# Kernel tuning notes

Measured on AMD Instinct MI355X. Metric: run time of the kernel, lower is better.

The kernel has to match this reference:

```python
import jax, jax.numpy as jnp
import numpy as np

B, H, W = 8, 56, 56
DIM, DIM_OUT, NUM_HEADS = 96, 192, 3
Q_STRIDE = (2, 2)


def setup_inputs() -> dict:
    key = jax.random.key(0)
    k1, k2, k3 = jax.random.split(key, 3)
    x = jax.random.normal(k1, (B, H, W, DIM), dtype=jnp.float32)
    W_qkv = jax.random.normal(k2, (DIM, 3 * DIM_OUT), dtype=jnp.float32) * 0.02
    b_qkv = jnp.zeros((3 * DIM_OUT,), dtype=jnp.float32)
    W_proj = jax.random.normal(k3, (DIM_OUT, DIM_OUT), dtype=jnp.float32) * 0.02
    b_proj = jnp.zeros((DIM_OUT,), dtype=jnp.float32)
    return {"x": x, "W_qkv": W_qkv, "b_qkv": b_qkv, "W_proj": W_proj, "b_proj": b_proj}


def reference(x, W_qkv, b_qkv, W_proj, b_proj):
    b, h, w, _ = x.shape
    c = W_proj.shape[0]          # dim_out
    nh = NUM_HEADS
    hd = c // nh                 # head_dim
    sh, sw = Q_STRIDE

    # fused QKV projection: (B,H,W,3*C)
    qkv = jnp.einsum("bhwd,de->bhwe", x, W_qkv) + b_qkv
    qkv = qkv.reshape(b, h * w, 3, nh, hd)
    q, k, v = qkv[:, :, 0], qkv[:, :, 1], qkv[:, :, 2]  # each (B,N,nh,hd)

    # query max-pool over spatial dims (channels = nh*hd, heads interleaved as in original)
    q = q.reshape(b, h, w, c)
    q = q.reshape(b, h // sh, sh, w // sw, sw, c).max(axis=(2, 4))  # (B,H',W',C)
    hn, wn = h // sh, w // sw
    q = q.reshape(b, hn * wn, nh, hd)

    # heads-first layout, scaled q
    q = q.transpose(0, 2, 1, 3) / jnp.sqrt(jnp.asarray(hd, x.dtype))  # (B,nh,Nq,hd)
    k = k.transpose(0, 2, 1, 3)                                       # (B,nh,Nk,hd)
    v = v.transpose(0, 2, 1, 3)

    attn = jax.nn.softmax(jnp.einsum("bnqd,bnkd->bnqk", q, k), axis=-1)
    out = jnp.einsum("bnqk,bnkd->bnqd", attn, v)        # (B,nh,Nq,hd)
    out = out.transpose(0, 2, 1, 3).reshape(b, hn, wn, c)

    return jnp.einsum("bhwc,cd->bhwd", out, W_proj) + b_proj
```

## Files before the change

### kernel.cpp

```cpp
#include <hip/hip_runtime.h>

#define BB    8
#define E3    576
#define DIMO  192
#define NH    3
#define HD    64
#define NK    3136
#define NQ    784
#define M1    25088
#define M2    6272
#define KSPLIT 7
#define KSLICE 448

typedef __bf16 bf16x8 __attribute__((ext_vector_type(8)));
typedef float f32x4  __attribute__((ext_vector_type(4)));

__device__ inline unsigned short f2bf(float f) {
    unsigned int u = __builtin_bit_cast(unsigned int, f);
    u += 0x7FFFu + ((u >> 16) & 1u);
    return (unsigned short)(u >> 16);
}

__global__ void wb_kernel(const float* __restrict__ Wqkv, unsigned short* __restrict__ Wb) {
    __shared__ float Ls[96][33];
    const int t = threadIdx.x;
    const int n0 = blockIdx.x * 32;
    int rr = t >> 5, c = t & 31;
#pragma unroll
    for (int rb = 0; rb < 12; ++rb) {
        int row = rb * 8 + rr;
        Ls[row][c] = Wqkv[(size_t)row * 576 + n0 + c];
    }
    __syncthreads();
    int n = t >> 3, kc = (t & 7) * 12;
#pragma unroll
    for (int j = 0; j < 12; j += 4) {
        ushort4 u = { f2bf(Ls[kc + j][n]), f2bf(Ls[kc + j + 1][n]),
                      f2bf(Ls[kc + j + 2][n]), f2bf(Ls[kc + j + 3][n]) };
        *(ushort4*)(Wb + (size_t)(n0 + n) * 96 + kc + j) = u;
    }
}

__launch_bounds__(256)
__global__ void qkv_mfma(const float* __restrict__ x,
                         const unsigned short* __restrict__ Wb,
                         const float* __restrict__ bias,
                         float* __restrict__ Qtmp,
                         unsigned short* __restrict__ Kb,
                         unsigned short* __restrict__ Vt) {
    __shared__ unsigned short xs[64 * 104];
    const int tid = threadIdx.x;
    const int wave = tid >> 6, lane = tid & 63;
    const int quad = lane >> 4, l16 = lane & 15;
    const int ntile = blockIdx.x;
    const int m0 = blockIdx.y * 64;

#pragma unroll
    for (int i = 0; i < 6; ++i) {
        int f = tid + i * 256;
        int r = f / 24, c4 = f % 24;
        float4 v = ((const float4*)x)[(size_t)(m0 + r) * 24 + c4];
        ushort4 u = { f2bf(v.x), f2bf(v.y), f2bf(v.z), f2bf(v.w) };
        *(ushort4*)&xs[r * 104 + c4 * 4] = u;
    }
    __syncthreads();

    f32x4 acc[12];
#pragma unroll
    for (int i = 0; i < 12; ++i) acc[i] = (f32x4){0.f, 0.f, 0.f, 0.f};

    const unsigned short* wb = Wb + (size_t)(ntile * 192 + l16) * 96 + quad * 8;
#pragma unroll
    for (int ch = 0; ch < 3; ++ch) {
        bf16x8 af = *(const bf16x8*)&xs[(wave * 16 + l16) * 104 + ch * 32 + quad * 8];
#pragma unroll
        for (int nf = 0; nf < 12; ++nf) {
            bf16x8 bfr = *(const bf16x8*)(wb + (size_t)nf * 16 * 96 + ch * 32);
            acc[nf] = __builtin_amdgcn_mfma_f32_16x16x32_bf16(af, bfr, acc[nf], 0, 0, 0);
        }
    }

    const int mbase = m0 + wave * 16 + quad * 4;
    if (ntile == 0) {
#pragma unroll
        for (int nf = 0; nf < 12; ++nf) {
            int n = nf * 16 + l16;
            float bs = bias[n];
#pragma unroll
            for (int i = 0; i < 4; ++i)
                Qtmp[(size_t)(mbase + i) * 192 + n] = acc[nf][i] + bs;
        }
    } else if (ntile == 1) {
#pragma unroll
        for (int nf = 0; nf < 12; ++nf) {
            int n = nf * 16 + l16;
            float bs = bias[192 + n];
#pragma unroll
            for (int i = 0; i < 4; ++i)
                Kb[(size_t)(mbase + i) * 192 + n] = f2bf(acc[nf][i] + bs);
        }
    } else {
        int b = m0 / NK;
        int key = mbase - b * NK;
#pragma unroll
        for (int nf = 0; nf < 12; ++nf) {
            int n = nf * 16 + l16;
            float bs = bias[384 + n];
            int hh = n >> 6, dd = n & 63;
            ushort4 u = { f2bf(acc[nf][0] + bs), f2bf(acc[nf][1] + bs),
                          f2bf(acc[nf][2] + bs), f2bf(acc[nf][3] + bs) };
            *(ushort4*)(Vt + ((size_t)((b * 3 + hh) * 64 + dd)) * NK + key) = u;
        }
    }
}

__global__ void qpool_bf16(const float* __restrict__ Qtmp, unsigned short* __restrict__ Qpb) {
    int idx = blockIdx.x * 256 + threadIdx.x;
    int d  = idx & 63;
    int q  = (idx >> 6) % NQ;
    int bh = idx / (64 * NQ);
    int b = bh / NH, h = bh % NH;
    int hq = q / 28, wq = q % 28;
    const float* base = Qtmp + (size_t)b * NK * 192 + h * 64 + d;
    int r0 = (2 * hq) * 56 + 2 * wq;
    float m = base[(size_t)r0 * 192];
    m = fmaxf(m, base[(size_t)(r0 + 1) * 192]);
    m = fmaxf(m, base[(size_t)(r0 + 56) * 192]);
    m = fmaxf(m, base[(size_t)(r0 + 57) * 192]);
    Qpb[idx] = f2bf(m * 0.125f);
}

__launch_bounds__(256)
__global__ void attn_mfma(const unsigned short* __restrict__ Qpb,
                          const unsigned short* __restrict__ Kb,
                          const unsigned short* __restrict__ Vt,
                          float* __restrict__ Pnum,
                          float* __restrict__ Pden) {
    __shared__ unsigned short Ks[64 * 88];
    __shared__ unsigned short Vs[64 * 88];
    __shared__ unsigned short Ps[4 * 32 * 88];

    const int tid = threadIdx.x;
    const int wave = tid >> 6, lane = tid & 63;
    const int quad = lane >> 4, l16 = lane & 15;
    const int bh = blockIdx.y, b = bh / NH, h = bh % NH;
    const int qt = blockIdx.x * 128 + wave * 32;
    const int ks = blockIdx.z, k00 = ks * KSLICE;

    const int srow0 = tid >> 3, sch = (tid & 7) * 8;
    const unsigned short* kg  = Kb + ((size_t)(b * NK + k00) + srow0) * DIMO + h * 64 + sch;
    const unsigned short* kg1 = kg + (size_t)32 * DIMO;
    const unsigned short* vg  = Vt + ((size_t)bh * 64 + srow0) * NK + k00 + sch;
    const unsigned short* vg1 = vg + (size_t)32 * NK;

    uint4 kp0 = *(const uint4*)kg;
    uint4 kp1 = *(const uint4*)kg1;
    uint4 vp0 = *(const uint4*)vg;
    uint4 vp1 = *(const uint4*)vg1;

    int qa = min(qt + l16, NQ - 1);
    int qb = min(qt + 16 + l16, NQ - 1);
    const unsigned short* qpa = Qpb + ((size_t)bh * NQ + qa) * HD + quad * 8;
    const unsigned short* qpc = Qpb + ((size_t)bh * NQ + qb) * HD + quad * 8;
    bf16x8 qf[2][2];
    qf[0][0] = *(const bf16x8*)qpa;  qf[0][1] = *(const bf16x8*)(qpa + 32);
    qf[1][0] = *(const bf16x8*)qpc;  qf[1][1] = *(const bf16x8*)(qpc + 32);

    const __bf16 one = (__bf16)1.0f;
    bf16x8 ones = { one, one, one, one, one, one, one, one };

    f32x4 on[4][2];
#pragma unroll
    for (int i = 0; i < 4; ++i)
#pragma unroll
        for (int j = 0; j < 2; ++j) on[i][j] = (f32x4){0.f, 0.f, 0.f, 0.f};
    f32x4 dn[2];
    dn[0] = (f32x4){0.f, 0.f, 0.f, 0.f};
    dn[1] = (f32x4){0.f, 0.f, 0.f, 0.f};

    unsigned short* myP = Ps + wave * 32 * 88;

    for (int s = 0; s < 7; ++s) {
        __syncthreads();
        *(uint4*)&Ks[srow0 * 88 + sch]        = kp0;
        *(uint4*)&Ks[(srow0 + 32) * 88 + sch] = kp1;
        *(uint4*)&Vs[srow0 * 88 + sch]        = vp0;
        *(uint4*)&Vs[(srow0 + 32) * 88 + sch] = vp1;
        __syncthreads();
        if (s < 6) {
            kp0 = *(const uint4*)(kg  + (size_t)(s + 1) * 64 * DIMO);
            kp1 = *(const uint4*)(kg1 + (size_t)(s + 1) * 64 * DIMO);
            vp0 = *(const uint4*)(vg  + (s + 1) * 64);
            vp1 = *(const uint4*)(vg1 + (s + 1) * 64);
        }

#pragma unroll
        for (int ksub = 0; ksub < 4; ++ksub) {
            bf16x8 kf0 = *(const bf16x8*)&Ks[(ksub * 16 + l16) * 88 + quad * 8];
            bf16x8 kf1 = *(const bf16x8*)&Ks[(ksub * 16 + l16) * 88 + 32 + quad * 8];
#pragma unroll
            for (int qsub = 0; qsub < 2; ++qsub) {
                f32x4 sa = (f32x4){0.f, 0.f, 0.f, 0.f};
                sa = __builtin_amdgcn_mfma_f32_16x16x32_bf16(kf0, qf[qsub][0], sa, 0, 0, 0);
                sa = __builtin_amdgcn_mfma_f32_16x16x32_bf16(kf1, qf[qsub][1], sa, 0, 0, 0);
                ushort4 pw = { f2bf(__expf(sa[0])), f2bf(__expf(sa[1])),
                               f2bf(__expf(sa[2])), f2bf(__expf(sa[3])) };
                *(ushort4*)&myP[(qsub * 16 + l16) * 88 + ksub * 16 + quad * 4] = pw;
            }
        }

#pragma unroll
        for (int k32 = 0; k32 < 2; ++k32) {
            bf16x8 pf0 = *(const bf16x8*)&myP[l16 * 88 + k32 * 32 + quad * 8];
            bf16x8 pf1 = *(const bf16x8*)&myP[(16 + l16) * 88 + k32 * 32 + quad * 8];
            dn[0] = __builtin_amdgcn_mfma_f32_16x16x32_bf16(ones, pf0, dn[0], 0, 0, 0);
            dn[1] = __builtin_amdgcn_mfma_f32_16x16x32_bf16(ones, pf1, dn[1], 0, 0, 0);
#pragma unroll
            for (int dsub = 0; dsub < 4; ++dsub) {
                bf16x8 vf = *(const bf16x8*)&Vs[(dsub * 16 + l16) * 88 + k32 * 32 + quad * 8];
                on[dsub][0] = __builtin_amdgcn_mfma_f32_16x16x32_bf16(vf, pf0, on[dsub][0], 0, 0, 0);
                on[dsub][1] = __builtin_amdgcn_mfma_f32_16x16x32_bf16(vf, pf1, on[dsub][1], 0, 0, 0);
            }
        }
    }

#pragma unroll
    for (int qsub = 0; qsub < 2; ++qsub) {
        int q = qt + qsub * 16 + l16;
        if (q < NQ) {
            size_t base = (size_t)ks * (24 * NQ * HD) + ((size_t)bh * NQ + q) * HD + quad * 4;
#pragma unroll
            for (int dsub = 0; dsub < 4; ++dsub)
                *(f32x4*)(Pnum + base + dsub * 16) = on[dsub][qsub];
            if (quad == 0) Pden[ks * (24 * NQ) + bh * NQ + q] = dn[qsub][0];
        }
    }
}

__global__ void combine_kernel(const float* __restrict__ Pnum,
                               const float* __restrict__ Pden,
                               float* __restrict__ AO) {
    int idx = blockIdx.x * 256 + threadIdx.x;
    int d = idx & 63;
    int rest = idx >> 6;
    int qq = rest % NQ;
    int bh = rest / NQ;
    int b = bh / NH, h = bh % NH;
    float num = 0.f, den = 0.f;
#pragma unroll
    for (int s = 0; s < KSPLIT; ++s) {
        num += Pnum[(size_t)s * (24 * NQ * HD) + idx];
        den += Pden[s * (24 * NQ) + bh * NQ + qq];
    }
    AO[((size_t)b * NQ + qq) * DIMO + h * 64 + d] = num / den;
}

template<int K, int LDB>
__launch_bounds__(256)
__global__ void gemm_kernel(const float* __restrict__ A,
                            const float* __restrict__ B,
                            const float* __restrict__ bias,
                            float* __restrict__ C) {
    constexpr int KT = 96;
    __shared__ float As[32][KT + 4];
    __shared__ float Bs[KT][64];

    const int tid = threadIdx.x;
    const int bm = blockIdx.y * 32;
    const int bn = blockIdx.x * 64;
    const int tx = tid & 15;
    const int ty = tid >> 4;

    float4 acc0 = {0.f, 0.f, 0.f, 0.f};
    float4 acc1 = {0.f, 0.f, 0.f, 0.f};

    for (int k0 = 0; k0 < K; k0 += KT) {
#pragma unroll
        for (int i = 0; i < 3; ++i) {
            int f = tid + i * 256;
            int r = f / 24, c = f % 24;
            float4 v = ((const float4*)A)[(size_t)(bm + r) * (K / 4) + (k0 / 4) + c];
            ((float4*)&As[r][0])[c] = v;
        }
#pragma unroll
        for (int i = 0; i < 6; ++i) {
            int f = tid + i * 256;
            int r = f >> 4, c = f & 15;
            float4 v = ((const float4*)B)[(size_t)(k0 + r) * (LDB / 4) + (bn >> 2) + c];
            ((float4*)&Bs[r][0])[c] = v;
        }
        __syncthreads();

#pragma unroll 8
        for (int k = 0; k < KT; ++k) {
            float a0 = As[ty][k];
            float a1 = As[ty + 16][k];
            float4 bb = ((const float4*)&Bs[k][0])[tx];
            acc0.x = fmaf(a0, bb.x, acc0.x);
            acc0.y = fmaf(a0, bb.y, acc0.y);
            acc0.z = fmaf(a0, bb.z, acc0.z);
            acc0.w = fmaf(a0, bb.w, acc0.w);
            acc1.x = fmaf(a1, bb.x, acc1.x);
            acc1.y = fmaf(a1, bb.y, acc1.y);
            acc1.z = fmaf(a1, bb.z, acc1.z);
            acc1.w = fmaf(a1, bb.w, acc1.w);
        }
        __syncthreads();
    }

    float4 bb = ((const float4*)bias)[(bn >> 2) + tx];
    acc0.x += bb.x; acc0.y += bb.y; acc0.z += bb.z; acc0.w += bb.w;
    acc1.x += bb.x; acc1.y += bb.y; acc1.z += bb.z; acc1.w += bb.w;

    ((float4*)C)[(size_t)(bm + ty) * (LDB / 4) + (bn >> 2) + tx] = acc0;
    ((float4*)C)[(size_t)(bm + ty + 16) * (LDB / 4) + (bn >> 2) + tx] = acc1;
}

extern "C" void kernel_launch(void* const* d_in, const int* in_sizes, int n_in,
                              void* d_out, int out_size, void* d_ws, size_t ws_size,
                              hipStream_t stream) {
    const float* x     = (const float*)d_in[0];
    const float* Wqkv  = (const float*)d_in[1];
    const float* bqkv  = (const float*)d_in[2];
    const float* Wproj = (const float*)d_in[3];
    const float* bproj = (const float*)d_in[4];
    float* out = (float*)d_out;

    float* Qtmp = (float*)d_ws;
    float* Pnum = Qtmp + (size_t)M1 * 192;
    float* Pden = Pnum + (size_t)KSPLIT * 24 * NQ * HD;
    float* AO   = Pden + (size_t)KSPLIT * 24 * NQ;
    unsigned short* Qpb = (unsigned short*)(AO + (size_t)M2 * DIMO);
    unsigned short* Kb  = Qpb + (size_t)24 * NQ * HD;
    unsigned short* Vt  = Kb + (size_t)BB * NK * DIMO;
    unsigned short* Wb  = Vt + (size_t)24 * HD * NK;

    wb_kernel<<<18, 256, 0, stream>>>(Wqkv, Wb);

    qkv_mfma<<<dim3(3, M1 / 64), 256, 0, stream>>>(x, Wb, bqkv, Qtmp, Kb, Vt);

    qpool_bf16<<<(24 * NQ * HD) / 256, 256, 0, stream>>>(Qtmp, Qpb);

    attn_mfma<<<dim3(7, 24, KSPLIT), 256, 0, stream>>>(Qpb, Kb, Vt, Pnum, Pden);

    combine_kernel<<<(24 * NQ * HD) / 256, 256, 0, stream>>>(Pnum, Pden, AO);

    gemm_kernel<192, 192><<<dim3(3, 196), 256, 0, stream>>>(AO, Wproj, bproj, out);
}
```

Before: 148.4 us.

## Use bf16 MFMA for output projection and compute softmax denominator in registers

The fp32 scalar-FMA output projection GEMM is replaced by a bf16 MFMA kernel. The combine kernel now writes bf16 attention output, and a merged prep kernel converts W_proj to transposed bf16. In attention, the denominator is summed from fp32 exponentials in registers with a cross-lane shuffle instead of extra MFMAs against a ones vector. The P tile shrinks to a 32-column half with a smaller stride, so PV runs per half. This trades some precision in the projection for fewer instructions and smaller LDS use.

```diff
diff --git a/kernel.cpp b/kernel.cpp
--- a/kernel.cpp
+++ b/kernel.cpp
@@ -11,6 +11,7 @@
 #define M2    6272
 #define KSPLIT 7
 #define KSLICE 448
+#define PSTR  56
 
 typedef __bf16 bf16x8 __attribute__((ext_vector_type(8)));
 typedef float f32x4  __attribute__((ext_vector_type(4)));
@@ -21,23 +22,42 @@
     return (unsigned short)(u >> 16);
 }
 
-__global__ void wb_kernel(const float* __restrict__ Wqkv, unsigned short* __restrict__ Wb) {
-    __shared__ float Ls[96][33];
+__global__ void wprep(const float* __restrict__ Wqkv, const float* __restrict__ Wproj,
+                      unsigned short* __restrict__ Wb, unsigned short* __restrict__ Wpb) {
+    __shared__ float Ls[192][33];
     const int t = threadIdx.x;
-    const int n0 = blockIdx.x * 32;
-    int rr = t >> 5, c = t & 31;
-#pragma unroll
-    for (int rb = 0; rb < 12; ++rb) {
-        int row = rb * 8 + rr;
-        Ls[row][c] = Wqkv[(size_t)row * 576 + n0 + c];
-    }
-    __syncthreads();
-    int n = t >> 3, kc = (t & 7) * 12;
-#pragma unroll
-    for (int j = 0; j < 12; j += 4) {
-        ushort4 u = { f2bf(Ls[kc + j][n]), f2bf(Ls[kc + j + 1][n]),
-                      f2bf(Ls[kc + j + 2][n]), f2bf(Ls[kc + j + 3][n]) };
-        *(ushort4*)(Wb + (size_t)(n0 + n) * 96 + kc + j) = u;
+    if (blockIdx.x < 18) {
+        const int n0 = blockIdx.x * 32;
+        int rr = t >> 5, c = t & 31;
+#pragma unroll
+        for (int rb = 0; rb < 12; ++rb) {
+            int row = rb * 8 + rr;
+            Ls[row][c] = Wqkv[(size_t)row * 576 + n0 + c];
+        }
+        __syncthreads();
+        int n = t >> 3, kc = (t & 7) * 12;
+#pragma unroll
+        for (int j = 0; j < 12; j += 4) {
+            ushort4 u = { f2bf(Ls[kc + j][n]), f2bf(Ls[kc + j + 1][n]),
+                          f2bf(Ls[kc + j + 2][n]), f2bf(Ls[kc + j + 3][n]) };
+            *(ushort4*)(Wb + (size_t)(n0 + n) * 96 + kc + j) = u;
+        }
+    } else {
+        const int n0 = (blockIdx.x - 18) * 32;
+        int rr = t >> 5, c = t & 31;
+#pragma unroll
+        for (int rb = 0; rb < 24; ++rb) {
+            int row = rb * 8 + rr;
+            Ls[row][c] = Wproj[(size_t)row * 192 + n0 + c];
+        }
+        __syncthreads();
+        int n = t >> 3, kc = (t & 7) * 24;
+#pragma unroll
+        for (int j = 0; j < 24; j += 4) {
+            ushort4 u = { f2bf(Ls[kc + j][n]), f2bf(Ls[kc + j + 1][n]),
+                          f2bf(Ls[kc + j + 2][n]), f2bf(Ls[kc + j + 3][n]) };
+            *(ushort4*)(Wpb + (size_t)(n0 + n) * 192 + kc + j) = u;
+        }
     }
 }
 
@@ -48,7 +68,7 @@
                          float* __restrict__ Qtmp,
                          unsigned short* __restrict__ Kb,
                          unsigned short* __restrict__ Vt) {
-    __shared__ unsigned short xs[64 * 104];
+    __shared__ __attribute__((aligned(16))) unsigned short xs[64 * 104];
     const int tid = threadIdx.x;
     const int wave = tid >> 6, lane = tid & 63;
     const int quad = lane >> 4, l16 = lane & 15;
@@ -136,9 +156,9 @@
                           const unsigned short* __restrict__ Vt,
                           float* __restrict__ Pnum,
                           float* __restrict__ Pden) {
-    __shared__ unsigned short Ks[64 * 88];
-    __shared__ unsigned short Vs[64 * 88];
-    __shared__ unsigned short Ps[4 * 32 * 88];
+    __shared__ __attribute__((aligned(16))) unsigned short Ks[64 * 88];
+    __shared__ __attribute__((aligned(16))) unsigned short Vs[64 * 88];
+    __shared__ __attribute__((aligned(16))) unsigned short Ps[4 * 32 * PSTR];
 
     const int tid = threadIdx.x;
     const int wave = tid >> 6, lane = tid & 63;
@@ -166,19 +186,14 @@
     qf[0][0] = *(const bf16x8*)qpa;  qf[0][1] = *(const bf16x8*)(qpa + 32);
     qf[1][0] = *(const bf16x8*)qpc;  qf[1][1] = *(const bf16x8*)(qpc + 32);
 
-    const __bf16 one = (__bf16)1.0f;
-    bf16x8 ones = { one, one, one, one, one, one, one, one };
-
     f32x4 on[4][2];
 #pragma unroll
     for (int i = 0; i < 4; ++i)
 #pragma unroll
         for (int j = 0; j < 2; ++j) on[i][j] = (f32x4){0.f, 0.f, 0.f, 0.f};
-    f32x4 dn[2];
-    dn[0] = (f32x4){0.f, 0.f, 0.f, 0.f};
-    dn[1] = (f32x4){0.f, 0.f, 0.f, 0.f};
-
-    unsigned short* myP = Ps + wave * 32 * 88;
+    float dden0 = 0.f, dden1 = 0.f;
+
+    unsigned short* myP = Ps + wave * 32 * PSTR;
 
     for (int s = 0; s < 7; ++s) {
         __syncthreads();
@@ -195,29 +210,30 @@
         }
 
 #pragma unroll
-        for (int ksub = 0; ksub < 4; ++ksub) {
-            bf16x8 kf0 = *(const bf16x8*)&Ks[(ksub * 16 + l16) * 88 + quad * 8];
-            bf16x8 kf1 = *(const bf16x8*)&Ks[(ksub * 16 + l16) * 88 + 32 + quad * 8];
-#pragma unroll
-            for (int qsub = 0; qsub < 2; ++qsub) {
-                f32x4 sa = (f32x4){0.f, 0.f, 0.f, 0.f};
-                sa = __builtin_amdgcn_mfma_f32_16x16x32_bf16(kf0, qf[qsub][0], sa, 0, 0, 0);
-                sa = __builtin_amdgcn_mfma_f32_16x16x32_bf16(kf1, qf[qsub][1], sa, 0, 0, 0);
-                ushort4 pw = { f2bf(__expf(sa[0])), f2bf(__expf(sa[1])),
-                               f2bf(__expf(sa[2])), f2bf(__expf(sa[3])) };
-                *(ushort4*)&myP[(qsub * 16 + l16) * 88 + ksub * 16 + quad * 4] = pw;
+        for (int half = 0; half < 2; ++half) {
+#pragma unroll
+            for (int ksub = 0; ksub < 2; ++ksub) {
+                const int krow = (half * 32 + ksub * 16 + l16) * 88;
+                bf16x8 kf0 = *(const bf16x8*)&Ks[krow + quad * 8];
+                bf16x8 kf1 = *(const bf16x8*)&Ks[krow + 32 + quad * 8];
+#pragma unroll
+                for (int qsub = 0; qsub < 2; ++qsub) {
+                    f32x4 sa = (f32x4){0.f, 0.f, 0.f, 0.f};
+                    sa = __builtin_amdgcn_mfma_f32_16x16x32_bf16(kf0, qf[qsub][0], sa, 0, 0, 0);
+                    sa = __builtin_amdgcn_mfma_f32_16x16x32_bf16(kf1, qf[qsub][1], sa, 0, 0, 0);
+                    float p0 = __expf(sa[0]), p1 = __expf(sa[1]);
+                    float p2 = __expf(sa[2]), p3 = __expf(sa[3]);
+                    if (qsub == 0) dden0 += (p0 + p1) + (p2 + p3);
+                    else           dden1 += (p0 + p1) + (p2 + p3);
+                    ushort4 pw = { f2bf(p0), f2bf(p1), f2bf(p2), f2bf(p3) };
+                    *(ushort4*)&myP[(qsub * 16 + l16) * PSTR + ksub * 16 + quad * 4] = pw;
+                }
             }
-        }
-
-#pragma unroll
-        for (int k32 = 0; k32 < 2; ++k32) {
-            bf16x8 pf0 = *(const bf16x8*)&myP[l16 * 88 + k32 * 32 + quad * 8];
-            bf16x8 pf1 = *(const bf16x8*)&myP[(16 + l16) * 88 + k32 * 32 + quad * 8];
-            dn[0] = __builtin_amdgcn_mfma_f32_16x16x32_bf16(ones, pf0, dn[0], 0, 0, 0);
-            dn[1] = __builtin_amdgcn_mfma_f32_16x16x32_bf16(ones, pf1, dn[1], 0, 0, 0);
+            bf16x8 pf0 = *(const bf16x8*)&myP[l16 * PSTR + quad * 8];
+            bf16x8 pf1 = *(const bf16x8*)&myP[(16 + l16) * PSTR + quad * 8];
 #pragma unroll
             for (int dsub = 0; dsub < 4; ++dsub) {
-                bf16x8 vf = *(const bf16x8*)&Vs[(dsub * 16 + l16) * 88 + k32 * 32 + quad * 8];
+                bf16x8 vf = *(const bf16x8*)&Vs[(dsub * 16 + l16) * 88 + half * 32 + quad * 8];
                 on[dsub][0] = __builtin_amdgcn_mfma_f32_16x16x32_bf16(vf, pf0, on[dsub][0], 0, 0, 0);
                 on[dsub][1] = __builtin_amdgcn_mfma_f32_16x16x32_bf16(vf, pf1, on[dsub][1], 0, 0, 0);
             }
@@ -226,20 +242,23 @@
 
 #pragma unroll
     for (int qsub = 0; qsub < 2; ++qsub) {
+        float r = (qsub == 0) ? dden0 : dden1;
+        r += __shfl_xor(r, 16, 64);
+        r += __shfl_xor(r, 32, 64);
         int q = qt + qsub * 16 + l16;
         if (q < NQ) {
             size_t base = (size_t)ks * (24 * NQ * HD) + ((size_t)bh * NQ + q) * HD + quad * 4;
 #pragma unroll
             for (int dsub = 0; dsub < 4; ++dsub)
                 *(f32x4*)(Pnum + base + dsub * 16) = on[dsub][qsub];
-            if (quad == 0) Pden[ks * (24 * NQ) + bh * NQ + q] = dn[qsub][0];
+            if (quad == 0) Pden[ks * (24 * NQ) + bh * NQ + q] = r;
         }
     }
 }
 
 __global__ void combine_kernel(const float* __restrict__ Pnum,
                                const float* __restrict__ Pden,
-                               float* __restrict__ AO) {
+                               unsigned short* __restrict__ AObf) {
     int idx = blockIdx.x * 256 + threadIdx.x;
     int d = idx & 63;
     int rest = idx >> 6;
@@ -252,68 +271,53 @@
         num += Pnum[(size_t)s * (24 * NQ * HD) + idx];
         den += Pden[s * (24 * NQ) + bh * NQ + qq];
     }
-    AO[((size_t)b * NQ + qq) * DIMO + h * 64 + d] = num / den;
-}
-
-template<int K, int LDB>
+    AObf[((size_t)b * NQ + qq) * DIMO + h * 64 + d] = f2bf(num / den);
+}
+
 __launch_bounds__(256)
-__global__ void gemm_kernel(const float* __restrict__ A,
-                            const float* __restrict__ B,
-                            const float* __restrict__ bias,
-                            float* __restrict__ C) {
-    constexpr int KT = 96;
-    __shared__ float As[32][KT + 4];
-    __shared__ float Bs[KT][64];
-
+__global__ void proj_mfma(const unsigned short* __restrict__ AObf,
+                          const unsigned short* __restrict__ Wpb,
+                          const float* __restrict__ bproj,
+                          float* __restrict__ out) {
+    __shared__ __attribute__((aligned(16))) unsigned short as_[64 * 200];
     const int tid = threadIdx.x;
-    const int bm = blockIdx.y * 32;
-    const int bn = blockIdx.x * 64;
-    const int tx = tid & 15;
-    const int ty = tid >> 4;
-
-    float4 acc0 = {0.f, 0.f, 0.f, 0.f};
-    float4 acc1 = {0.f, 0.f, 0.f, 0.f};
-
-    for (int k0 = 0; k0 < K; k0 += KT) {
-#pragma unroll
-        for (int i = 0; i < 3; ++i) {
-            int f = tid + i * 256;
-            int r = f / 24, c = f % 24;
-            float4 v = ((const float4*)A)[(size_t)(bm + r) * (K / 4) + (k0 / 4) + c];
-            ((float4*)&As[r][0])[c] = v;
-        }
-#pragma unroll
-        for (int i = 0; i < 6; ++i) {
-            int f = tid + i * 256;
-            int r = f >> 4, c = f & 15;
-            float4 v = ((const float4*)B)[(size_t)(k0 + r) * (LDB / 4) + (bn >> 2) + c];
-            ((float4*)&Bs[r][0])[c] = v;
-        }
-        __syncthreads();
-
-#pragma unroll 8
-        for (int k = 0; k < KT; ++k) {
-            float a0 = As[ty][k];
-            float a1 = As[ty + 16][k];
-            float4 bb = ((const float4*)&Bs[k][0])[tx];
-            acc0.x = fmaf(a0, bb.x, acc0.x);
-            acc0.y = fmaf(a0, bb.y, acc0.y);
-            acc0.z = fmaf(a0, bb.z, acc0.z);
-            acc0.w = fmaf(a0, bb.w, acc0.w);
-            acc1.x = fmaf(a1, bb.x, acc1.x);
-            acc1.y = fmaf(a1, bb.y, acc1.y);
-            acc1.z = fmaf(a1, bb.z, acc1.z);
-            acc1.w = fmaf(a1, bb.w, acc1.w);
-        }
-        __syncthreads();
-    }
-
-    float4 bb = ((const float4*)bias)[(bn >> 2) + tx];
-    acc0.x += bb.x; acc0.y += bb.y; acc0.z += bb.z; acc0.w += bb.w;
-    acc1.x += bb.x; acc1.y += bb.y; acc1.z += bb.z; acc1.w += bb.w;
-
-    ((float4*)C)[(size_t)(bm + ty) * (LDB / 4) + (bn >> 2) + tx] = acc0;
-    ((float4*)C)[(size_t)(bm + ty + 16) * (LDB / 4) + (bn >> 2) + tx] = acc1;
+    const int wave = tid >> 6, lane = tid & 63;
+    const int quad = lane >> 4, l16 = lane & 15;
+    const int ntile = blockIdx.x;
+    const int m0 = blockIdx.y * 64;
+
+#pragma unroll
+    for (int i = 0; i < 6; ++i) {
+        int f = tid + i * 256;
+        int r = f / 24, c = f % 24;
+        *(uint4*)&as_[r * 200 + c * 8] = *(const uint4*)(AObf + (size_t)(m0 + r) * 192 + c * 8);
+    }
+    __syncthreads();
+
+    f32x4 acc[4];
+#pragma unroll
+    for (int i = 0; i < 4; ++i) acc[i] = (f32x4){0.f, 0.f, 0.f, 0.f};
+
+    const unsigned short* wp = Wpb + (size_t)(ntile * 64 + l16) * 192 + quad * 8;
+#pragma unroll
+    for (int ch = 0; ch < 6; ++ch) {
+        bf16x8 af = *(const bf16x8*)&as_[(wave * 16 + l16) * 200 + ch * 32 + quad * 8];
+#pragma unroll
+        for (int nf = 0; nf < 4; ++nf) {
+            bf16x8 bfr = *(const bf16x8*)(wp + (size_t)nf * 16 * 192 + ch * 32);
+            acc[nf] = __builtin_amdgcn_mfma_f32_16x16x32_bf16(af, bfr, acc[nf], 0, 0, 0);
+        }
+    }
+
+    const int m = m0 + wave * 16 + quad * 4;
+#pragma unroll
+    for (int nf = 0; nf < 4; ++nf) {
+        int n = ntile * 64 + nf * 16 + l16;
+        float bs = bproj[n];
+#pragma unroll
+        for (int i = 0; i < 4; ++i)
+            out[(size_t)(m + i) * 192 + n] = acc[nf][i] + bs;
+    }
 }
 
 extern "C" void kernel_launch(void* const* d_in, const int* in_sizes, int n_in,
@@ -329,13 +333,14 @@
     float* Qtmp = (float*)d_ws;
     float* Pnum = Qtmp + (size_t)M1 * 192;
     float* Pden = Pnum + (size_t)KSPLIT * 24 * NQ * HD;
-    float* AO   = Pden + (size_t)KSPLIT * 24 * NQ;
-    unsigned short* Qpb = (unsigned short*)(AO + (size_t)M2 * DIMO);
+    unsigned short* AObf = (unsigned short*)(Pden + (size_t)KSPLIT * 24 * NQ);
+    unsigned short* Qpb = AObf + (size_t)M2 * DIMO;
     unsigned short* Kb  = Qpb + (size_t)24 * NQ * HD;
     unsigned short* Vt  = Kb + (size_t)BB * NK * DIMO;
     unsigned short* Wb  = Vt + (size_t)24 * HD * NK;
-
-    wb_kernel<<<18, 256, 0, stream>>>(Wqkv, Wb);
+    unsigned short* Wpb = Wb + (size_t)576 * 96;
+
+    wprep<<<24, 256, 0, stream>>>(Wqkv, Wproj, Wb, Wpb);
 
     qkv_mfma<<<dim3(3, M1 / 64), 256, 0, stream>>>(x, Wb, bqkv, Qtmp, Kb, Vt);
 
@@ -343,7 +348,7 @@
 
     attn_mfma<<<dim3(7, 24, KSPLIT), 256, 0, stream>>>(Qpb, Kb, Vt, Pnum, Pden);
 
-    combine_kernel<<<(24 * NQ * HD) / 256, 256, 0, stream>>>(Pnum, Pden, AO);
-
-    gemm_kernel<192, 192><<<dim3(3, 196), 256, 0, stream>>>(AO, Wproj, bproj, out);
-}
+    combine_kernel<<<(24 * NQ * HD) / 256, 256, 0, stream>>>(Pnum, Pden, AObf);
+
+    proj_mfma<<<dim3(3, M2 / 64), 256, 0, stream>>>(AObf, Wpb, bproj, out);
+}
```

Result: no change. 145.9 us (-1.7%).
